# Kernel tuning notes

Measured on AMD Instinct MI355X. Metric: run time of the kernel, lower is better.

The kernel has to match this reference:

```python
import jax, jax.numpy as jnp
import numpy as np

B, S, D, E, H = 65536, 4, 128, 128, 4
HD = E // H
EPS = 1e-5


def setup_inputs() -> dict:
    key = jax.random.key(0)
    ks = jax.random.split(key, 20)
    sc = 0.05
    return {
        'h0': jax.random.normal(ks[0], (B, D), jnp.float32),
        'h1': jax.random.normal(ks[1], (B, D), jnp.float32),
        'h2': jax.random.normal(ks[2], (B, D), jnp.float32),
        'h3': jax.random.normal(ks[3], (B, D), jnp.float32),
        'proj_w': jax.random.normal(ks[4], (S, D, E), jnp.float32) * sc,
        'proj_b': jax.random.normal(ks[5], (S, E), jnp.float32) * sc,
        'ctx_w': jax.random.normal(ks[6], (E,), jnp.float32) * sc,
        'ctx_b': jax.random.normal(ks[7], (), jnp.float32) * sc,
        'in_proj_w': jax.random.normal(ks[8], (E, 3 * E), jnp.float32) * sc,
        'in_proj_b': jax.random.normal(ks[9], (3 * E,), jnp.float32) * sc,
        'out_w': jax.random.normal(ks[10], (E, E), jnp.float32) * sc,
        'out_b': jax.random.normal(ks[11], (E,), jnp.float32) * sc,
        'gate_w': jax.random.normal(ks[12], (2 * E, E), jnp.float32) * sc,
        'gate_b': jax.random.normal(ks[13], (E,), jnp.float32) * sc,
        'pool_w': jax.random.normal(ks[14], (E,), jnp.float32) * sc,
        'pool_b': jax.random.normal(ks[15], (), jnp.float32) * sc,
        'ln_g': jnp.ones((E,), jnp.float32),
        'ln_b': jnp.zeros((E,), jnp.float32),
    }


def reference(h0, h1, h2, h3, proj_w, proj_b, ctx_w, ctx_b, in_proj_w, in_proj_b,
              out_w, out_b, gate_w, gate_b, pool_w, pool_b, ln_g, ln_b):
    hs = jnp.stack([h0, h1, h2, h3], axis=1)                      # [B,S,D]
    x = jnp.einsum('bsd,sde->bse', hs, proj_w) + proj_b           # [B,S,E]
    # context attention over sources
    cw = jax.nn.softmax(x @ ctx_w + ctx_b, axis=1)                # [B,S]
    context = jnp.einsum('bse,bs->be', x, cw)                     # [B,E]
    # single-query MHA: query=context, keys/vals=x
    wq, wk, wv = jnp.split(in_proj_w, 3, axis=1)
    bq, bk, bv = jnp.split(in_proj_b, 3)
    q = (context @ wq + bq).reshape(B, H, HD)
    k = (x @ wk + bk).reshape(B, S, H, HD)
    v = (x @ wv + bv).reshape(B, S, H, HD)
    scores = jnp.einsum('bhd,bshd->bhs', q, k) / jnp.sqrt(jnp.float32(HD))
    attn = jax.nn.softmax(scores, axis=-1)                        # [B,H,S]
    o = jnp.einsum('bhs,bshd->bhd', attn, v).reshape(B, E)
    attn_out = o @ out_w + out_b                                  # [B,E]
    attn_weights = jnp.mean(attn, axis=1)[:, None, :]             # [B,1,S] (avg heads)
    ao = jnp.broadcast_to(attn_out[:, None, :], (B, S, E))
    gate_in = jnp.concatenate([x, ao], axis=-1)                   # [B,S,2E]
    g = jax.nn.sigmoid(gate_in @ gate_w + gate_b)                 # [B,S,E]
    fused = g * ao + (1.0 - g) * x
    mu = fused.mean(axis=-1, keepdims=True)
    var = fused.var(axis=-1, keepdims=True)
    fused = (fused - mu) * jax.lax.rsqrt(var + EPS) * ln_g + ln_b
    pw = jax.nn.softmax(fused @ pool_w + pool_b, axis=1)          # [B,S]
    pooled = jnp.einsum('bse,bs->be', fused, pw)                  # [B,E]
    return pooled, attn_weights, g
```

## Files before the change

kernel.cpp:

```cpp
#include <hip/hip_runtime.h>
#include <hip/hip_bf16.h>

typedef unsigned short u16;
typedef unsigned int   u32;
typedef short  short8 __attribute__((ext_vector_type(8)));
typedef float  f32x4  __attribute__((ext_vector_type(4)));

#define NB    65536
#define XP    132
#define OFF1  ((size_t)NB * 128)
#define OFF2  (OFF1 + (size_t)NB * 4)

__device__ __forceinline__ u16 f2bf(float f) {
  __hip_bfloat16 b = __float2bfloat16(f);
  u16 u; __builtin_memcpy(&u, &b, 2); return u;
}
__device__ __forceinline__ float bf2f(u32 bits16) {
  union { u32 u; float f; } v; v.u = bits16 << 16; return v.f;
}
__device__ __forceinline__ u32 pk2(float a, float b) {
  return (u32)f2bf(a) | ((u32)f2bf(b) << 16);
}
__device__ __forceinline__ float unpk(u32 w, int hi) {
  return bf2f(hi ? (w >> 16) : (w & 0xffffu));
}
__device__ __forceinline__ float red16(float v) {
  v += __shfl_xor(v, 1); v += __shfl_xor(v, 2);
  v += __shfl_xor(v, 4); v += __shfl_xor(v, 8);
  return v;
}
__device__ __forceinline__ void lds_fence() {
  asm volatile("s_waitcnt lgkmcnt(0)" ::: "memory");
}

__global__ void pack_w(const float* __restrict__ proj_w,
                       const float* __restrict__ in_proj_w,
                       const float* __restrict__ out_w,
                       const float* __restrict__ gate_w,
                       u16* __restrict__ wp) {
  int t = blockIdx.x * 256 + threadIdx.x;
  if (t >= 10 * 16384) return;
  int w = t >> 14, i = t & 16383;
  int nt = i >> 11, kt = (i >> 9) & 3, ln = (i >> 3) & 63, j = i & 7;
  int k = kt * 32 + ((ln >> 4) << 3) + j;
  int n = (nt << 4) + (ln & 15);
  float v;
  if (w < 4)       v = proj_w[((size_t)w << 14) + (k << 7) + n];
  else if (w < 7)  v = in_proj_w[k * 384 + ((w - 4) << 7) + n];
  else if (w == 7) v = out_w[(k << 7) + n];
  else             v = gate_w[(((w - 8) << 7) + k) * 128 + n];
  wp[t] = f2bf(v);
}

__device__ __forceinline__ short8 bfrag(const u16* __restrict__ wp, int w, int nt, int kt, int lane) {
  return *(const short8*)(wp + ((size_t)w << 14) + (size_t)((((nt << 2) + kt) << 6) + lane) * 8);
}

struct AF { short8 a[4]; };
__device__ __forceinline__ AF loadA(const u16 (*Ab)[XP], int row, int lgrp) {
  AF r;
  #pragma unroll
  for (int kt = 0; kt < 4; ++kt)
    r.a[kt] = *(const short8*)&Ab[row][kt * 32 + (lgrp << 3)];
  return r;
}
__device__ __forceinline__ f32x4 mmK128(const AF& A, const u16* __restrict__ wp, int w,
                                        int ntg, int lane, float bias) {
  f32x4 acc = {bias, bias, bias, bias};
  #pragma unroll
  for (int kt = 0; kt < 4; ++kt)
    acc = __builtin_amdgcn_mfma_f32_16x16x32_bf16(A.a[kt], bfrag(wp, w, ntg, kt, lane), acc, 0, 0, 0);
  return acc;
}

__global__ __launch_bounds__(256) void fused_k(
    const float* __restrict__ h0, const float* __restrict__ h1,
    const float* __restrict__ h2, const float* __restrict__ h3,
    const u16* __restrict__ wp,
    const float* __restrict__ proj_b, const float* __restrict__ ctx_w,
    const float* __restrict__ in_proj_b, const float* __restrict__ out_b,
    const float* __restrict__ gate_b, const float* __restrict__ pool_w,
    const float* __restrict__ ln_g, const float* __restrict__ ln_b,
    float* __restrict__ out) {
  __shared__ __align__(16) u16 xls4[4][3][16][XP];
  __shared__ __align__(16) u16 scr4[4][16][XP];

  const int tid   = threadIdx.x;
  const int lane  = tid & 63;
  const int wid   = tid >> 6;
  const int lrow  = lane & 15;
  const int lgrp  = lane >> 4;
  const int crow0 = lgrp << 2;
  const size_t r0w = ((size_t)blockIdx.x * 4 + wid) * 16;

  u16 (*xls)[16][XP] = xls4[wid];
  u16 (*scr)[XP]     = scr4[wid];

  const float* hp[4] = {h0, h1, h2, h3};

  float ctxl[4][4];
  AF Axs[4];
  u32 xcp0[8][2];
  #pragma unroll
  for (int s = 0; s < 4; ++s) {
    const float* __restrict__ hb = hp[s] + ((r0w + lrow) << 7) + (lgrp << 3);
    AF Ah;
    #pragma unroll
    for (int kt = 0; kt < 4; ++kt) {
      f32x4 va = __builtin_nontemporal_load((const f32x4*)(hb + kt * 32));
      f32x4 vb = __builtin_nontemporal_load((const f32x4*)(hb + kt * 32 + 4));
      u32 tmp[4] = {pk2(va[0], va[1]), pk2(va[2], va[3]), pk2(vb[0], vb[1]), pk2(vb[2], vb[3])};
      __builtin_memcpy(&Ah.a[kt], tmp, 16);
    }
    float lp[4] = {0.f, 0.f, 0.f, 0.f};
    #pragma unroll
    for (int nt = 0; nt < 8; ++nt) {
      int n = (nt << 4) + lrow;
      f32x4 acc = mmK128(Ah, wp, s, nt, lane, proj_b[(s << 7) + n]);
      float cwn = ctx_w[n];
      #pragma unroll
      for (int j = 0; j < 4; ++j) {
        lp[j] += acc[j] * cwn;
        if (s == 0) scr[crow0 + j][n] = f2bf(acc[j]);
        else        xls[s - 1][crow0 + j][n] = f2bf(acc[j]);
      }
      if (s == 0) {
        xcp0[nt][0] = pk2(acc[0], acc[1]);
        xcp0[nt][1] = pk2(acc[2], acc[3]);
      }
    }
    #pragma unroll
    for (int j = 0; j < 4; ++j) ctxl[s][j] = red16(lp[j]);
    if (s == 0) {
      lds_fence();
      Axs[0] = loadA(scr, lrow, lgrp);
    }
  }

  float cw[4][4];
  #pragma unroll
  for (int j = 0; j < 4; ++j) {
    float l0 = ctxl[0][j], l1 = ctxl[1][j], l2 = ctxl[2][j], l3 = ctxl[3][j];
    float mx = fmaxf(fmaxf(l0, l1), fmaxf(l2, l3));
    float e0 = __expf(l0 - mx), e1 = __expf(l1 - mx), e2 = __expf(l2 - mx), e3 = __expf(l3 - mx);
    float inv = 1.f / (e0 + e1 + e2 + e3);
    cw[0][j] = e0 * inv; cw[1][j] = e1 * inv; cw[2][j] = e2 * inv; cw[3][j] = e3 * inv;
  }
  #pragma unroll
  for (int nt = 0; nt < 8; ++nt) {
    int n = (nt << 4) + lrow;
    #pragma unroll
    for (int j = 0; j < 4; ++j) {
      float v = cw[0][j] * unpk(xcp0[nt][j >> 1], j & 1)
              + cw[1][j] * bf2f((u32)xls[0][crow0 + j][n])
              + cw[2][j] * bf2f((u32)xls[1][crow0 + j][n])
              + cw[3][j] * bf2f((u32)xls[2][crow0 + j][n]);
      scr[crow0 + j][n] = f2bf(v);
    }
  }
  lds_fence();
  AF Ac = loadA(scr, lrow, lgrp);

  float qf[8][4];
  #pragma unroll
  for (int nt = 0; nt < 8; ++nt) {
    int n = (nt << 4) + lrow;
    f32x4 acc = mmK128(Ac, wp, 4, nt, lane, in_proj_b[n]);
    #pragma unroll
    for (int j = 0; j < 4; ++j) qf[nt][j] = acc[j];
  }

  lds_fence();
  #pragma unroll
  for (int s = 1; s < 4; ++s) Axs[s] = loadA(xls[s - 1], lrow, lgrp);
  float sc[4][4][4] = {};
  #pragma unroll
  for (int nt = 0; nt < 8; ++nt) {
    int n = (nt << 4) + lrow;
    const int h = nt >> 1;
    float bk = in_proj_b[128 + n];
    f32x4 ak[4];
    #pragma unroll
    for (int s = 0; s < 4; ++s) ak[s] = (f32x4){bk, bk, bk, bk};
    #pragma unroll
    for (int kt = 0; kt < 4; ++kt) {
      short8 bf = bfrag(wp, 5, nt, kt, lane);
      #pragma unroll
      for (int s = 0; s < 4; ++s)
        ak[s] = __builtin_amdgcn_mfma_f32_16x16x32_bf16(Axs[s].a[kt], bf, ak[s], 0, 0, 0);
    }
    #pragma unroll
    for (int s = 0; s < 4; ++s)
      #pragma unroll
      for (int j = 0; j < 4; ++j)
        sc[s][j][h] += ak[s][j] * qf[nt][j];
  }
  #pragma unroll
  for (int s = 0; s < 4; ++s)
    #pragma unroll
    for (int j = 0; j < 4; ++j)
      #pragma unroll
      for (int h = 0; h < 4; ++h)
        sc[s][j][h] = red16(sc[s][j][h]);

  float aw[4][4][4];
  #pragma unroll
  for (int j = 0; j < 4; ++j)
    #pragma unroll
    for (int h = 0; h < 4; ++h) {
      const float scale = 0.17677669529663687f;
      float l0 = sc[0][j][h] * scale, l1 = sc[1][j][h] * scale;
      float l2 = sc[2][j][h] * scale, l3 = sc[3][j][h] * scale;
      float mx = fmaxf(fmaxf(l0, l1), fmaxf(l2, l3));
      float e0 = __expf(l0 - mx), e1 = __expf(l1 - mx), e2 = __expf(l2 - mx), e3 = __expf(l3 - mx);
      float inv = 1.f / (e0 + e1 + e2 + e3);
      aw[0][j][h] = e0 * inv; aw[1][j][h] = e1 * inv;
      aw[2][j][h] = e2 * inv; aw[3][j][h] = e3 * inv;
    }
  {
    float* awp = (float*)scr;
    if (lrow == 0) {
      #pragma unroll
      for (int s = 0; s < 4; ++s)
        #pragma unroll
        for (int j = 0; j < 4; ++j)
          awp[((crow0 + j) << 2) + s] =
            0.25f * (aw[s][j][0] + aw[s][j][1] + aw[s][j][2] + aw[s][j][3]);
    }
    lds_fence();
    __builtin_nontemporal_store(awp[lane], &out[OFF1 + (r0w << 2) + lane]);
  }

  {
    float oa[8][4] = {};
    #pragma unroll
    for (int nt = 0; nt < 8; ++nt) {
      int n = (nt << 4) + lrow;
      const int h = nt >> 1;
      float bv = in_proj_b[256 + n];
      f32x4 av[4];
      #pragma unroll
      for (int s = 0; s < 4; ++s) av[s] = (f32x4){bv, bv, bv, bv};
      #pragma unroll
      for (int kt = 0; kt < 4; ++kt) {
        short8 bf = bfrag(wp, 6, nt, kt, lane);
        #pragma unroll
        for (int s = 0; s < 4; ++s)
          av[s] = __builtin_amdgcn_mfma_f32_16x16x32_bf16(Axs[s].a[kt], bf, av[s], 0, 0, 0);
      }
      #pragma unroll
      for (int s = 0; s < 4; ++s)
        #pragma unroll
        for (int j = 0; j < 4; ++j)
          oa[nt][j] += aw[s][j][h] * av[s][j];
    }
    #pragma unroll
    for (int nt = 0; nt < 8; ++nt) {
      int n = (nt << 4) + lrow;
      #pragma unroll
      for (int j = 0; j < 4; ++j) scr[crow0 + j][n] = f2bf(oa[nt][j]);
    }
  }
  lds_fence();
  AF Ao = loadA(scr, lrow, lgrp);

  float aoreg[8][4];
  #pragma unroll
  for (int nt = 0; nt < 8; ++nt) {
    int n = (nt << 4) + lrow;
    f32x4 acc = mmK128(Ao, wp, 7, nt, lane, out_b[n]);
    #pragma unroll
    for (int j = 0; j < 4; ++j) {
      scr[crow0 + j][n] = f2bf(acc[j]);
      aoreg[nt][j] = acc[j];
    }
  }
  lds_fence();
  AF Aa = loadA(scr, lrow, lgrp);

  f32x4 aacc[8];
  #pragma unroll
  for (int nt = 0; nt < 8; ++nt) {
    int n = (nt << 4) + lrow;
    float gb = gate_b[n];
    f32x4 t = {gb, gb, gb, gb};
    #pragma unroll
    for (int kt = 0; kt < 4; ++kt)
      t = __builtin_amdgcn_mfma_f32_16x16x32_bf16(Aa.a[kt], bfrag(wp, 9, nt, kt, lane), t, 0, 0, 0);
    aacc[nt] = t;
  }
  float sm[4][4] = {}, sq[4][4] = {};
  #pragma unroll
  for (int nt = 0; nt < 8; ++nt) {
    int n = (nt << 4) + lrow;
    short8 bf8[4];
    #pragma unroll
    for (int kt = 0; kt < 4; ++kt) bf8[kt] = bfrag(wp, 8, nt, kt, lane);
    #pragma unroll
    for (int s = 0; s < 4; ++s) {
      f32x4 acc = aacc[nt];
      #pragma unroll
      for (int kt = 0; kt < 4; ++kt)
        acc = __builtin_amdgcn_mfma_f32_16x16x32_bf16(Axs[s].a[kt], bf8[kt], acc, 0, 0, 0);
      float f[4];
      #pragma unroll
      for (int j = 0; j < 4; ++j) {
        float g = 1.f / (1.f + __expf(-acc[j]));
        __builtin_nontemporal_store(g, &out[OFF2 + (((r0w + crow0 + j) << 2) + s) * 128 + n]);
        float xv = (s == 0) ? unpk(xcp0[nt][j >> 1], j & 1)
                            : bf2f((u32)xls[s - 1][crow0 + j][n]);
        f[j] = g * aoreg[nt][j] + (1.f - g) * xv;
        sm[s][j] += f[j];
        sq[s][j] += f[j] * f[j];
        if (s > 0) xls[s - 1][crow0 + j][n] = f2bf(f[j]);
      }
      if (s == 0) {
        xcp0[nt][0] = pk2(f[0], f[1]);
        xcp0[nt][1] = pk2(f[2], f[3]);
      }
    }
  }
  float mean_[4][4], rstd_[4][4];
  #pragma unroll
  for (int s = 0; s < 4; ++s)
    #pragma unroll
    for (int j = 0; j < 4; ++j) {
      float ts = red16(sm[s][j]);
      float tq = red16(sq[s][j]);
      float mean = ts * 0.0078125f;
      float var  = tq * 0.0078125f - mean * mean;
      mean_[s][j] = mean;
      rstd_[s][j] = rsqrtf(var + 1e-5f);
    }

  float lngv[8], lnbv[8], pwvv[8];
  #pragma unroll
  for (int nt = 0; nt < 8; ++nt) {
    int n = (nt << 4) + lrow;
    lngv[nt] = ln_g[n]; lnbv[nt] = ln_b[n]; pwvv[nt] = pool_w[n];
  }
  float pp[4][4] = {};
  #pragma unroll
  for (int nt = 0; nt < 8; ++nt) {
    int n = (nt << 4) + lrow;
    #pragma unroll
    for (int s = 0; s < 4; ++s)
      #pragma unroll
      for (int j = 0; j < 4; ++j) {
        float f  = (s == 0) ? unpk(xcp0[nt][j >> 1], j & 1)
                            : bf2f((u32)xls[s - 1][crow0 + j][n]);
        float fn = (f - mean_[s][j]) * rstd_[s][j] * lngv[nt] + lnbv[nt];
        pp[s][j] += fn * pwvv[nt];
      }
  }
  float pw[4][4];
  #pragma unroll
  for (int j = 0; j < 4; ++j) {
    float l0 = red16(pp[0][j]), l1 = red16(pp[1][j]);
    float l2 = red16(pp[2][j]), l3 = red16(pp[3][j]);
    float mx = fmaxf(fmaxf(l0, l1), fmaxf(l2, l3));
    float e0 = __expf(l0 - mx), e1 = __expf(l1 - mx), e2 = __expf(l2 - mx), e3 = __expf(l3 - mx);
    float inv = 1.f / (e0 + e1 + e2 + e3);
    pw[0][j] = e0 * inv; pw[1][j] = e1 * inv; pw[2][j] = e2 * inv; pw[3][j] = e3 * inv;
  }
  #pragma unroll
  for (int nt = 0; nt < 8; ++nt) {
    int n = (nt << 4) + lrow;
    #pragma unroll
    for (int j = 0; j < 4; ++j) {
      float acc = 0.f;
      #pragma unroll
      for (int s = 0; s < 4; ++s) {
        float f  = (s == 0) ? unpk(xcp0[nt][j >> 1], j & 1)
                            : bf2f((u32)xls[s - 1][crow0 + j][n]);
        float fn = (f - mean_[s][j]) * rstd_[s][j] * lngv[nt] + lnbv[nt];
        acc += pw[s][j] * fn;
      }
      __builtin_nontemporal_store(acc, &out[((r0w + crow0 + j) << 7) + n]);
    }
  }
}

extern "C" void kernel_launch(void* const* d_in, const int* in_sizes, int n_in,
                              void* d_out, int out_size, void* d_ws, size_t ws_size,
                              hipStream_t stream) {
  const float* h0        = (const float*)d_in[0];
  const float* h1        = (const float*)d_in[1];
  const float* h2        = (const float*)d_in[2];
  const float* h3        = (const float*)d_in[3];
  const float* proj_w    = (const float*)d_in[4];
  const float* proj_b    = (const float*)d_in[5];
  const float* ctx_w     = (const float*)d_in[6];
  const float* in_proj_w = (const float*)d_in[8];
  const float* in_proj_b = (const float*)d_in[9];
  const float* out_w     = (const float*)d_in[10];
  const float* out_b     = (const float*)d_in[11];
  const float* gate_w    = (const float*)d_in[12];
  const float* gate_b    = (const float*)d_in[13];
  const float* pool_w    = (const float*)d_in[14];
  const float* ln_g      = (const float*)d_in[16];
  const float* ln_b      = (const float*)d_in[17];
  u16* wp = (u16*)d_ws;

  pack_w<<<640, 256, 0, stream>>>(proj_w, in_proj_w, out_w, gate_w, wp);
  fused_k<<<NB / 64, 256, 0, stream>>>(h0, h1, h2, h3, wp,
                                       proj_b, ctx_w, in_proj_b, out_b, gate_b,
                                       pool_w, ln_g, ln_b, (float*)d_out);
}
```

Baseline: 198.7 us.

## Stage packed weight matrices into LDS with double-buffered async global-to-LDS loads

Each of the ten packed bf16 weight matrices is copied into a 64 KB double-buffered LDS area with global_load_lds. The copy of the next matrix is issued while the current matrix is consumed, and MFMA B-fragments are then read from LDS instead of from global memory. The aim is to stop every wave from re-reading the same weights through the vector memory path and L1/L2. The cost is a block-wide __syncthreads at each stage and a much larger LDS footprint, which likely cuts resident blocks per CU and so reduces latency hiding.

```diff
diff --git a/kernel.cpp b/kernel.cpp
--- a/kernel.cpp
+++ b/kernel.cpp
@@ -31,6 +31,12 @@
 }
 __device__ __forceinline__ void lds_fence() {
   asm volatile("s_waitcnt lgkmcnt(0)" ::: "memory");
+}
+
+typedef __attribute__((address_space(1))) u32 gu32;
+typedef __attribute__((address_space(3))) u32 lu32;
+__device__ __forceinline__ void gld_lds16(const u16* g, u16* l) {
+  __builtin_amdgcn_global_load_lds((gu32*)g, (lu32*)l, 16, 0, 0);
 }
 
 __global__ void pack_w(const float* __restrict__ proj_w,
@@ -52,8 +58,8 @@
   wp[t] = f2bf(v);
 }
 
-__device__ __forceinline__ short8 bfrag(const u16* __restrict__ wp, int w, int nt, int kt, int lane) {
-  return *(const short8*)(wp + ((size_t)w << 14) + (size_t)((((nt << 2) + kt) << 6) + lane) * 8);
+__device__ __forceinline__ short8 bfragL(const u16* wb, int nt, int kt, int lane) {
+  return *(const short8*)(wb + (size_t)((((nt << 2) + kt) << 6) + lane) * 8);
 }
 
 struct AF { short8 a[4]; };
@@ -64,12 +70,12 @@
     r.a[kt] = *(const short8*)&Ab[row][kt * 32 + (lgrp << 3)];
   return r;
 }
-__device__ __forceinline__ f32x4 mmK128(const AF& A, const u16* __restrict__ wp, int w,
-                                        int ntg, int lane, float bias) {
+__device__ __forceinline__ f32x4 mmK128L(const AF& A, const u16* wb,
+                                         int ntg, int lane, float bias) {
   f32x4 acc = {bias, bias, bias, bias};
   #pragma unroll
   for (int kt = 0; kt < 4; ++kt)
-    acc = __builtin_amdgcn_mfma_f32_16x16x32_bf16(A.a[kt], bfrag(wp, w, ntg, kt, lane), acc, 0, 0, 0);
+    acc = __builtin_amdgcn_mfma_f32_16x16x32_bf16(A.a[kt], bfragL(wb, ntg, kt, lane), acc, 0, 0, 0);
   return acc;
 }
 
@@ -82,6 +88,7 @@
     const float* __restrict__ gate_b, const float* __restrict__ pool_w,
     const float* __restrict__ ln_g, const float* __restrict__ ln_b,
     float* __restrict__ out) {
+  __shared__ __align__(16) u16 wbuf[2][16384];
   __shared__ __align__(16) u16 xls4[4][3][16][XP];
   __shared__ __align__(16) u16 scr4[4][16][XP];
 
@@ -96,7 +103,19 @@
   u16 (*xls)[16][XP] = xls4[wid];
   u16 (*scr)[XP]     = scr4[wid];
 
+  auto stage_w = [&](int b, int w) {
+    const u16* src = wp + ((size_t)w << 14);
+    u16* dst = wbuf[b];
+    #pragma unroll
+    for (int i = 0; i < 8; ++i) {
+      int c = (wid << 3) + i;
+      gld_lds16(src + (c << 9) + (lane << 3), dst + (c << 9));
+    }
+  };
+
   const float* hp[4] = {h0, h1, h2, h3};
+
+  stage_w(0, 0);
 
   float ctxl[4][4];
   AF Axs[4];
@@ -112,11 +131,14 @@
       u32 tmp[4] = {pk2(va[0], va[1]), pk2(va[2], va[3]), pk2(vb[0], vb[1]), pk2(vb[2], vb[3])};
       __builtin_memcpy(&Ah.a[kt], tmp, 16);
     }
+    __syncthreads();
+    stage_w((s + 1) & 1, s + 1);
+    const u16* wb = wbuf[s & 1];
     float lp[4] = {0.f, 0.f, 0.f, 0.f};
     #pragma unroll
     for (int nt = 0; nt < 8; ++nt) {
       int n = (nt << 4) + lrow;
-      f32x4 acc = mmK128(Ah, wp, s, nt, lane, proj_b[(s << 7) + n]);
+      f32x4 acc = mmK128L(Ah, wb, nt, lane, proj_b[(s << 7) + n]);
       float cwn = ctx_w[n];
       #pragma unroll
       for (int j = 0; j < 4; ++j) {
@@ -161,15 +183,19 @@
   lds_fence();
   AF Ac = loadA(scr, lrow, lgrp);
 
+  __syncthreads();
+  stage_w(1, 5);
   float qf[8][4];
   #pragma unroll
   for (int nt = 0; nt < 8; ++nt) {
     int n = (nt << 4) + lrow;
-    f32x4 acc = mmK128(Ac, wp, 4, nt, lane, in_proj_b[n]);
+    f32x4 acc = mmK128L(Ac, wbuf[0], nt, lane, in_proj_b[n]);
     #pragma unroll
     for (int j = 0; j < 4; ++j) qf[nt][j] = acc[j];
   }
 
+  __syncthreads();
+  stage_w(0, 6);
   lds_fence();
   #pragma unroll
   for (int s = 1; s < 4; ++s) Axs[s] = loadA(xls[s - 1], lrow, lgrp);
@@ -184,7 +210,7 @@
     for (int s = 0; s < 4; ++s) ak[s] = (f32x4){bk, bk, bk, bk};
     #pragma unroll
     for (int kt = 0; kt < 4; ++kt) {
-      short8 bf = bfrag(wp, 5, nt, kt, lane);
+      short8 bf = bfragL(wbuf[1], nt, kt, lane);
       #pragma unroll
       for (int s = 0; s < 4; ++s)
         ak[s] = __builtin_amdgcn_mfma_f32_16x16x32_bf16(Axs[s].a[kt], bf, ak[s], 0, 0, 0);
@@ -231,6 +257,8 @@
     __builtin_nontemporal_store(awp[lane], &out[OFF1 + (r0w << 2) + lane]);
   }
 
+  __syncthreads();
+  stage_w(1, 7);
   {
     float oa[8][4] = {};
     #pragma unroll
@@ -243,7 +271,7 @@
       for (int s = 0; s < 4; ++s) av[s] = (f32x4){bv, bv, bv, bv};
       #pragma unroll
       for (int kt = 0; kt < 4; ++kt) {
-        short8 bf = bfrag(wp, 6, nt, kt, lane);
+        short8 bf = bfragL(wbuf[0], nt, kt, lane);
         #pragma unroll
         for (int s = 0; s < 4; ++s)
           av[s] = __builtin_amdgcn_mfma_f32_16x16x32_bf16(Axs[s].a[kt], bf, av[s], 0, 0, 0);
@@ -264,11 +292,13 @@
   lds_fence();
   AF Ao = loadA(scr, lrow, lgrp);
 
+  __syncthreads();
+  stage_w(0, 9);
   float aoreg[8][4];
   #pragma unroll
   for (int nt = 0; nt < 8; ++nt) {
     int n = (nt << 4) + lrow;
-    f32x4 acc = mmK128(Ao, wp, 7, nt, lane, out_b[n]);
+    f32x4 acc = mmK128L(Ao, wbuf[1], nt, lane, out_b[n]);
     #pragma unroll
     for (int j = 0; j < 4; ++j) {
       scr[crow0 + j][n] = f2bf(acc[j]);
@@ -278,6 +308,8 @@
   lds_fence();
   AF Aa = loadA(scr, lrow, lgrp);
 
+  __syncthreads();
+  stage_w(1, 8);
   f32x4 aacc[8];
   #pragma unroll
   for (int nt = 0; nt < 8; ++nt) {
@@ -286,16 +318,18 @@
     f32x4 t = {gb, gb, gb, gb};
     #pragma unroll
     for (int kt = 0; kt < 4; ++kt)
-      t = __builtin_amdgcn_mfma_f32_16x16x32_bf16(Aa.a[kt], bfrag(wp, 9, nt, kt, lane), t, 0, 0, 0);
+      t = __builtin_amdgcn_mfma_f32_16x16x32_bf16(Aa.a[kt], bfragL(wbuf[0], nt, kt, lane), t, 0, 0, 0);
     aacc[nt] = t;
   }
+
+  __syncthreads();
   float sm[4][4] = {}, sq[4][4] = {};
   #pragma unroll
   for (int nt = 0; nt < 8; ++nt) {
     int n = (nt << 4) + lrow;
     short8 bf8[4];
     #pragma unroll
-    for (int kt = 0; kt < 4; ++kt) bf8[kt] = bfrag(wp, 8, nt, kt, lane);
+    for (int kt = 0; kt < 4; ++kt) bf8[kt] = bfragL(wbuf[1], nt, kt, lane);
     #pragma unroll
     for (int s = 0; s < 4; ++s) {
       f32x4 acc = aacc[nt];
```

Result: faster. 191.2 us (-3.8%).
